# Kernel optimization log

Hardware: AMD Instinct MI355X
Metric: run time of the kernel (lower is better)

The kernel has to match this reference:

```python
import jax, jax.numpy as jnp
import numpy as np

DIM = 768
HEADS = 12
HEAD_DIM = DIM // HEADS
HIDDEN = 4 * DIM
EPS = 1e-5


def _ln(x, w, b):
    mu = jnp.mean(x, axis=-1, keepdims=True)
    var = jnp.var(x, axis=-1, keepdims=True)
    return (x - mu) * jax.lax.rsqrt(var + EPS) * w + b


def setup_inputs() -> dict:
    key = jax.random.key(0)
    ks = jax.random.split(key, 8)
    B, N, C = 8, 1024, DIM
    s = 0.02
    return {
        "before": jax.random.normal(ks[0], (B, N, C), jnp.float32),
        "after": jax.random.normal(ks[1], (B, N, C), jnp.float32),
        "norm1_w": jnp.ones((C,), jnp.float32),
        "norm1_b": jnp.zeros((C,), jnp.float32),
        "qkv_w": jax.random.normal(ks[2], (3 * C, C), jnp.float32) * s,
        "hln_w": jnp.ones((HEAD_DIM,), jnp.float32),
        "hln_b": jnp.zeros((HEAD_DIM,), jnp.float32),
        "proj_w": jax.random.normal(ks[3], (C, C), jnp.float32) * s,
        "proj_b": jnp.zeros((C,), jnp.float32),
        "norm2_w": jnp.ones((C,), jnp.float32),
        "norm2_b": jnp.zeros((C,), jnp.float32),
        "fc1_w": jax.random.normal(ks[4], (HIDDEN, C), jnp.float32) * s,
        "fc1_b": jnp.zeros((HIDDEN,), jnp.float32),
        "fc2_w": jax.random.normal(ks[5], (C, HIDDEN), jnp.float32) * s,
        "fc2_b": jnp.zeros((C,), jnp.float32),
    }


def _qkv_normed(x, qkv_w, hln_w, hln_b):
    B, N, C = x.shape
    qkv = x @ qkv_w.T  # (B,N,3C)
    qkv = qkv.reshape(B, N, 3, HEADS, HEAD_DIM).transpose(2, 0, 3, 1, 4)  # (3,B,H,N,hd)
    qkv = _ln(qkv, hln_w, hln_b)  # per-head LayerNorm over head_dim
    return qkv[0], qkv[1], qkv[2]


def _cross_attn(q, k, v, proj_w, proj_b):
    B, H, N, D = q.shape
    scale = D ** (-0.5)
    attn = jax.nn.softmax(jnp.einsum("bhnd,bhmd->bhnm", q, k) * scale, axis=-1)
    ctx = jnp.einsum("bhnm,bhmd->bhnd", attn, v)
    ctx = ctx.transpose(0, 2, 1, 3).reshape(B, N, H * D)
    ctx = ctx @ proj_w.T + proj_b
    # NOTE: original adds q.reshape(B,N,C) WITHOUT transposing heads (faithful)
    return ctx + q.reshape(B, N, H * D)


def _mlp(x, fc1_w, fc1_b, fc2_w, fc2_b):
    h = jax.nn.gelu(x @ fc1_w.T + fc1_b, approximate=False)
    return h @ fc2_w.T + fc2_b


def reference(before, after, norm1_w, norm1_b, qkv_w, hln_w, hln_b, proj_w, proj_b,
              norm2_w, norm2_b, fc1_w, fc1_b, fc2_w, fc2_b):
    before_n = _ln(before, norm1_w, norm1_b)
    after_n = _ln(after, norm1_w, norm1_b)
    q_b, k_b, v_b = _qkv_normed(before_n, qkv_w, hln_w, hln_b)
    q_a, k_a, v_a = _qkv_normed(after_n, qkv_w, hln_w, hln_b)
    context_a = _cross_attn(q_b, k_a, v_a, proj_w, proj_b)  # before attends to after
    context_b = _cross_attn(q_a, k_b, v_b, proj_w, proj_b)  # after attends to before
    before_o = before_n + context_b
    after_o = after_n + context_a
    before_o = before_o + _mlp(_ln(before_o, norm2_w, norm2_b), fc1_w, fc1_b, fc2_w, fc2_b)
    after_o = after_o + _mlp(_ln(after_o, norm2_w, norm2_b), fc1_w, fc1_b, fc2_w, fc2_b)
    return (before_o, after_o)
```

## Files before the change

### kernel.cpp

```cpp
#include <hip/hip_runtime.h>
#include <hip/hip_bf16.h>

typedef unsigned short u16;
typedef __attribute__((ext_vector_type(8))) short bf16x8;
typedef __attribute__((ext_vector_type(4))) float f32x4;

#define DIRSTRIDE 6291456

__device__ __forceinline__ u16 f2bf(float x){
  __hip_bfloat16 h = __float2bfloat16(x);
  return *reinterpret_cast<u16*>(&h);
}
__device__ __forceinline__ float bf2f(u16 u){
  return __uint_as_float(((unsigned int)u) << 16);
}
__device__ __forceinline__ u16 f2bf_fast(float x){
  return (u16)((__float_as_uint(x) + 0x8000u) >> 16);
}

__device__ __forceinline__ void xcd_remap(int& bx, int& by){
  int gx = (int)gridDim.x;
  int lin = (int)blockIdx.x + gx*(int)blockIdx.y;
  int nwg8 = (gx*(int)gridDim.y) >> 3;
  int rl = (lin & 7)*nwg8 + (lin >> 3);
  bx = rl % gx; by = rl / gx;
}

__global__ __launch_bounds__(256) void zero_kernel(float* __restrict__ p, int n){
  int i = blockIdx.x*256 + threadIdx.x;
  if (i < n) p[i] = 0.f;
}

__global__ __launch_bounds__(256) void cvt_kernel(const float* __restrict__ s,
                                                  u16* __restrict__ d, int n){
  int i = blockIdx.x*256 + threadIdx.x;
  if (i < n) d[i] = f2bf(s[i]);
}

__global__ __launch_bounds__(256) void ln_kernel(const float* __restrict__ s0,
    const float* __restrict__ s1, const float* __restrict__ w,
    const float* __restrict__ b, u16* __restrict__ out,
    float* __restrict__ mu_out, float* __restrict__ rs_out){
  int r = blockIdx.x;
  const float* src = (r < 8192) ? (s0 + (size_t)r*768) : (s1 + (size_t)(r-8192)*768);
  int t = threadIdx.x;
  float v0 = src[t], v1 = src[t+256], v2 = src[t+512];
  __shared__ float red[4];
  float s = v0+v1+v2;
  #pragma unroll
  for (int o=32;o;o>>=1) s += __shfl_xor(s,o);
  if ((t&63)==0) red[t>>6] = s;
  __syncthreads();
  float mean = (red[0]+red[1]+red[2]+red[3]) * (1.0f/768.0f);
  float d0=v0-mean, d1=v1-mean, d2=v2-mean;
  float q = d0*d0+d1*d1+d2*d2;
  __syncthreads();
  #pragma unroll
  for (int o=32;o;o>>=1) q += __shfl_xor(q,o);
  if ((t&63)==0) red[t>>6] = q;
  __syncthreads();
  float var = (red[0]+red[1]+red[2]+red[3]) * (1.0f/768.0f);
  float rstd = rsqrtf(var + 1e-5f);
  if (mu_out && t == 0){ mu_out[r] = mean; rs_out[r] = rstd; }
  size_t base = (size_t)r*768;
  out[base+t]     = f2bf(d0*rstd*w[t]     + b[t]);
  out[base+t+256] = f2bf(d1*rstd*w[t+256] + b[t+256]);
  out[base+t+512] = f2bf(d2*rstd*w[t+512] + b[t+512]);
}

__device__ __forceinline__ void stage_tile64(const u16* g, size_t strideK, u16* lds,
                                             int w, int lane){
  #pragma unroll
  for (int i=0;i<4;i++){
    int row = w*32 + i*8 + (lane>>3);
    int cs  = (lane&7) ^ (row&7);
    const u16* gp = g + (size_t)row*strideK + cs*8;
    __builtin_amdgcn_global_load_lds(
        (const __attribute__((address_space(1))) unsigned int*)gp,
        (__attribute__((address_space(3))) unsigned int*)(lds + (w*4+i)*512),
        16, 0, 0);
  }
}

__device__ __forceinline__ void stage_tile64x64(const u16* g, size_t strideK,
                                                u16* lds, int w, int lane){
  #pragma unroll
  for (int i=0;i<2;i++){
    int row = w*16 + i*8 + (lane>>3);
    int cs  = (lane&7) ^ (row&7);
    const u16* gp = g + (size_t)row*strideK + cs*8;
    __builtin_amdgcn_global_load_lds(
        (const __attribute__((address_space(1))) unsigned int*)gp,
        (__attribute__((address_space(3))) unsigned int*)(lds + (w*2+i)*512),
        16, 0, 0);
  }
}

#define SWZ_FRAG(tile, r, c) (*(const bf16x8*)&(tile)[(r)*64 + (((c) ^ ((r)&7)))*8])

template<int EPI>
__global__ __launch_bounds__(256, 4) void gemm_kernel(
    const u16* __restrict__ A, const u16* __restrict__ W, void* Cout,
    const float* __restrict__ bias, const float* resF,
    int M, int N, int K)
{
  __shared__ __attribute__((aligned(16))) u16 sA[128*64];
  __shared__ __attribute__((aligned(16))) u16 sB[128*64];
  int t = threadIdx.x;
  int w = t>>6, lane = t&63, ln = lane&15, quad = lane>>4;
  int bx, by; xcd_remap(bx, by);
  int m0 = by*128, n0 = bx*128;
  int wr = (w>>1)*64, wc = (w&1)*64;
  f32x4 acc[4][4];
  #pragma unroll
  for (int mi=0;mi<4;mi++)
    #pragma unroll
    for (int ni=0;ni<4;ni++) acc[mi][ni] = (f32x4){0.f,0.f,0.f,0.f};
  int KB = K >> 6;
  for (int kb=0;kb<KB;kb++){
    __syncthreads();
    stage_tile64(A + (size_t)m0*K + kb*64, K, sA, w, lane);
    stage_tile64(W + (size_t)n0*K + kb*64, K, sB, w, lane);
    __syncthreads();
    #pragma unroll
    for (int ks=0;ks<2;ks++){
      bf16x8 aF[4], bF[4];
      #pragma unroll
      for (int mi=0;mi<4;mi++) aF[mi] = SWZ_FRAG(sA, wr+mi*16+ln, ks*4+quad);
      #pragma unroll
      for (int ni=0;ni<4;ni++) bF[ni] = SWZ_FRAG(sB, wc+ni*16+ln, ks*4+quad);
      #pragma unroll
      for (int mi=0;mi<4;mi++)
        #pragma unroll
        for (int ni=0;ni<4;ni++)
          acc[mi][ni] = __builtin_amdgcn_mfma_f32_16x16x32_bf16(aF[mi], bF[ni], acc[mi][ni], 0,0,0);
    }
  }
  #pragma unroll
  for (int mi=0;mi<4;mi++){
    #pragma unroll
    for (int ni=0;ni<4;ni++){
      #pragma unroll
      for (int r=0;r<4;r++){
        int row = m0 + wr + mi*16 + quad*4 + r;
        int col = n0 + wc + ni*16 + ln;
        size_t ridx = (size_t)row*N + col;
        float v = acc[mi][ni][r];
        if (EPI == 2){
          v += bias[col];
          v = 0.5f*v*(1.0f + erff(v*0.70710678118654752f));
          ((u16*)Cout)[ridx] = f2bf(v);
        } else {
          float rf = resF[ridx];
          ((float*)Cout)[ridx] = v + bias[col] + rf;
        }
      }
    }
  }
}

__global__ __launch_bounds__(256, 4) void gemm_fc2_kernel(
    const u16* __restrict__ A, const u16* __restrict__ W, float* __restrict__ Cout,
    const float* __restrict__ bias, const float* resF)
{
  const int N = 768, K = 3072, KB = 48;
  __shared__ __attribute__((aligned(16))) u16 sA[128*64];
  __shared__ __attribute__((aligned(16))) u16 sB[64*64];
  int t = threadIdx.x;
  int w = t>>6, lane = t&63, ln = lane&15, quad = lane>>4;
  int bx, by; xcd_remap(bx, by);
  int m0 = by*128, n0 = bx*64;
  int wr = w*32;
  f32x4 acc[2][4];
  #pragma unroll
  for (int mi=0;mi<2;mi++)
    #pragma unroll
    for (int ni=0;ni<4;ni++) acc[mi][ni] = (f32x4){0.f,0.f,0.f,0.f};
  for (int kb=0;kb<KB;kb++){
    __syncthreads();
    stage_tile64(A + (size_t)m0*K + kb*64, K, sA, w, lane);
    stage_tile64x64(W + (size_t)n0*K + kb*64, K, sB, w, lane);
    __syncthreads();
    #pragma unroll
    for (int ks=0;ks<2;ks++){
      bf16x8 aF[2], bF[4];
      #pragma unroll
      for (int mi=0;mi<2;mi++) aF[mi] = SWZ_FRAG(sA, wr+mi*16+ln, ks*4+quad);
      #pragma unroll
      for (int ni=0;ni<4;ni++) bF[ni] = SWZ_FRAG(sB, ni*16+ln, ks*4+quad);
      #pragma unroll
      for (int mi=0;mi<2;mi++)
        #pragma unroll
        for (int ni=0;ni<4;ni++)
          acc[mi][ni] = __builtin_amdgcn_mfma_f32_16x16x32_bf16(aF[mi], bF[ni], acc[mi][ni], 0,0,0);
    }
  }
  #pragma unroll
  for (int mi=0;mi<2;mi++){
    #pragma unroll
    for (int ni=0;ni<4;ni++){
      #pragma unroll
      for (int r=0;r<4;r++){
        int row = m0 + wr + mi*16 + quad*4 + r;
        int col = n0 + ni*16 + ln;
        size_t ridx = (size_t)row*N + col;
        float rf = resF[ridx];
        Cout[ridx] = acc[mi][ni][r] + bias[col] + rf;
      }
    }
  }
}

__global__ __launch_bounds__(256, 4) void gemm_proj_kernel(
    const u16* __restrict__ A, const u16* __restrict__ W, float* Cout,
    const float* __restrict__ bias, const u16* __restrict__ resQ,
    const float* __restrict__ before, const float* __restrict__ after,
    const float* __restrict__ n1w, const float* __restrict__ n1b,
    const float* __restrict__ mu, const float* __restrict__ rstd)
{
  const int K = 768, N = 768, KB = 12;
  __shared__ __attribute__((aligned(16))) u16 sA[128*64];
  __shared__ __attribute__((aligned(16))) u16 sB[128*64];
  int t = threadIdx.x;
  int w = t>>6, lane = t&63, ln = lane&15, quad = lane>>4;
  int bx, by; xcd_remap(bx, by);
  int m0 = by*128, n0 = bx*128;
  int wr = (w>>1)*64, wc = (w&1)*64;
  f32x4 acc[4][4];
  #pragma unroll
  for (int mi=0;mi<4;mi++)
    #pragma unroll
    for (int ni=0;ni<4;ni++) acc[mi][ni] = (f32x4){0.f,0.f,0.f,0.f};
  for (int kb=0;kb<KB;kb++){
    __syncthreads();
    stage_tile64(A + (size_t)m0*K + kb*64, K, sA, w, lane);
    stage_tile64(W + (size_t)n0*K + kb*64, K, sB, w, lane);
    __syncthreads();
    #pragma unroll
    for (int ks=0;ks<2;ks++){
      bf16x8 aF[4], bF[4];
      #pragma unroll
      for (int mi=0;mi<4;mi++) aF[mi] = SWZ_FRAG(sA, wr+mi*16+ln, ks*4+quad);
      #pragma unroll
      for (int ni=0;ni<4;ni++) bF[ni] = SWZ_FRAG(sB, wc+ni*16+ln, ks*4+quad);
      #pragma unroll
      for (int mi=0;mi<4;mi++)
        #pragma unroll
        for (int ni=0;ni<4;ni++)
          acc[mi][ni] = __builtin_amdgcn_mfma_f32_16x16x32_bf16(aF[mi], bF[ni], acc[mi][ni], 0,0,0);
    }
  }
  #pragma unroll
  for (int mi=0;mi<4;mi++){
    #pragma unroll
    for (int ni=0;ni<4;ni++){
      #pragma unroll
      for (int r=0;r<4;r++){
        int row = m0 + wr + mi*16 + quad*4 + r;
        int col = n0 + wc + ni*16 + ln;
        size_t ridx = (size_t)row*N + col;
        int dirout = row >> 13;
        int rem = row & 8191;
        size_t qidx = (size_t)(1-dirout)*DIRSTRIDE + (size_t)rem*768 + col;
        const float* src = dirout ? after : before;
        float xr = (src[(size_t)rem*768 + col] - mu[row]) * rstd[row] * n1w[col] + n1b[col];
        Cout[ridx] = acc[mi][ni][r] + bias[col] + bf2f(resQ[qidx]) + xr;
      }
    }
  }
}

__global__ __launch_bounds__(256, 4) void gemm_qkv_kernel(
    const u16* __restrict__ A, const u16* __restrict__ W,
    const float* __restrict__ hw, const float* __restrict__ hb,
    u16* __restrict__ q, u16* __restrict__ k, u16* __restrict__ vt)
{
  const int K = 768, KB = 12;
  __shared__ __attribute__((aligned(16))) u16 sA[128*64];
  __shared__ __attribute__((aligned(16))) u16 sB[128*64];
  int t = threadIdx.x;
  int w = t>>6, lane = t&63, ln = lane&15, quad = lane>>4;
  int bx, by; xcd_remap(bx, by);
  int m0 = by*128, n0 = bx*128;
  int wr = (w>>1)*64, wc = (w&1)*64;
  f32x4 acc[4][4];
  #pragma unroll
  for (int mi=0;mi<4;mi++)
    #pragma unroll
    for (int ni=0;ni<4;ni++) acc[mi][ni] = (f32x4){0.f,0.f,0.f,0.f};
  for (int kb=0;kb<KB;kb++){
    __syncthreads();
    stage_tile64(A + (size_t)m0*K + kb*64, K, sA, w, lane);
    stage_tile64(W + (size_t)n0*K + kb*64, K, sB, w, lane);
    __syncthreads();
    #pragma unroll
    for (int ks=0;ks<2;ks++){
      bf16x8 aF[4], bF[4];
      #pragma unroll
      for (int mi=0;mi<4;mi++) aF[mi] = SWZ_FRAG(sA, wr+mi*16+ln, ks*4+quad);
      #pragma unroll
      for (int ni=0;ni<4;ni++) bF[ni] = SWZ_FRAG(sB, wc+ni*16+ln, ks*4+quad);
      #pragma unroll
      for (int mi=0;mi<4;mi++)
        #pragma unroll
        for (int ni=0;ni<4;ni++)
          acc[mi][ni] = __builtin_amdgcn_mfma_f32_16x16x32_bf16(aF[mi], bF[ni], acc[mi][ni], 0,0,0);
    }
  }
  int sec = (n0 + wc) >> 6;
  int which = sec / 12, h = sec - which*12;
  float hwv[4], hbv[4];
  #pragma unroll
  for (int ni=0;ni<4;ni++){ hwv[ni] = hw[ni*16+ln]; hbv[ni] = hb[ni*16+ln]; }
  #pragma unroll
  for (int mi=0;mi<4;mi++){
    #pragma unroll
    for (int r=0;r<4;r++){
      float s = acc[mi][0][r]+acc[mi][1][r]+acc[mi][2][r]+acc[mi][3][r];
      #pragma unroll
      for (int ofs=1; ofs<16; ofs<<=1) s += __shfl_xor(s, ofs);
      float mu = s * (1.0f/64.0f);
      float vv = 0.f;
      #pragma unroll
      for (int ni=0;ni<4;ni++){ float d = acc[mi][ni][r]-mu; vv += d*d; }
      #pragma unroll
      for (int ofs=1; ofs<16; ofs<<=1) vv += __shfl_xor(vv, ofs);
      float rstd = rsqrtf(vv*(1.0f/64.0f) + 1e-5f);
      int token = m0 + wr + mi*16 + quad*4 + r;
      int dir = token >> 13, bb = (token>>10)&7, n = token & 1023;
      size_t base = (size_t)dir*DIRSTRIDE + (size_t)bb*786432 + (size_t)h*65536;
      #pragma unroll
      for (int ni=0;ni<4;ni++){
        u16 y = f2bf((acc[mi][ni][r]-mu)*rstd*hwv[ni] + hbv[ni]);
        int hd = ni*16 + ln;
        if (which == 0)      q[base + (size_t)n*64 + hd] = y;
        else if (which == 1) k[base + (size_t)n*64 + hd] = y;
        else                 vt[base + (size_t)hd*1024 + n] = y;
      }
    }
  }
}

__global__ __launch_bounds__(256) void flash_kernel(const u16* __restrict__ qg,
    const u16* __restrict__ kg, const u16* __restrict__ vtg, u16* __restrict__ ctx)
{
  __shared__ __attribute__((aligned(16))) u16 sK[2][64*64];
  __shared__ __attribute__((aligned(16))) u16 sV[2][64*64];
  __shared__ __attribute__((aligned(16))) u16 sP[4*32*72];
  int lin = (int)blockIdx.x + 8*((int)blockIdx.y + 96*(int)blockIdx.z);
  int x8 = lin & 7, jj = lin >> 3;
  int qt = jj & 7;
  int g  = x8 + 8*(jj >> 3);
  int dout = g & 1, bh = g >> 1;
  int b = bh/12, h = bh - b*12;
  size_t qbase = (size_t)(1-dout)*DIRSTRIDE + (size_t)b*786432 + (size_t)h*65536;
  size_t kbase = (size_t)dout*DIRSTRIDE + (size_t)b*786432 + (size_t)h*65536;
  int t = threadIdx.x;
  int w = t>>6, lane = t&63, ln = lane&15, quad = lane>>4;
  const u16* qp = qg + qbase + (size_t)(qt*128 + w*32 + ln)*64 + quad*8;
  bf16x8 aQ[2][2];
  aQ[0][0] = *(const bf16x8*)qp;
  aQ[0][1] = *(const bf16x8*)(qp + 32);
  aQ[1][0] = *(const bf16x8*)(qp + 16*64);
  aQ[1][1] = *(const bf16x8*)(qp + 16*64 + 32);
  bf16x8 vOne;
  #pragma unroll
  for (int j=0;j<8;j++) vOne[j] = (short)0x3F80;
  f32x4 o[2][4], oL[2];
  #pragma unroll
  for (int mi=0;mi<2;mi++){
    #pragma unroll
    for (int ni=0;ni<4;ni++) o[mi][ni] = (f32x4){0.f,0.f,0.f,0.f};
    oL[mi] = (f32x4){0.f,0.f,0.f,0.f};
  }
  u16* pw = &sP[w*32*72];
  const float cs = 0.18033688011112042f;
  stage_tile64x64(kg  + kbase, 64, sK[0], w, lane);
  stage_tile64x64(vtg + kbase, 1024, sV[0], w, lane);
  __syncthreads();
  int cur = 0;
  for (int kt=0;kt<16;kt++){
    if (kt < 15){
      stage_tile64x64(kg  + kbase + (size_t)(kt+1)*4096, 64, sK[cur^1], w, lane);
      stage_tile64x64(vtg + kbase + (size_t)(kt+1)*64, 1024, sV[cur^1], w, lane);
    }
    const u16* sKc = sK[cur];
    const u16* sVc = sV[cur];
    bf16x8 bK[4][2];
    #pragma unroll
    for (int ni=0;ni<4;ni++){
      int rr = ni*16 + ln;
      bK[ni][0] = SWZ_FRAG(sKc, rr, quad);
      bK[ni][1] = SWZ_FRAG(sKc, rr, 4+quad);
    }
    f32x4 s[2][4];
    __builtin_amdgcn_s_setprio(1);
    #pragma unroll
    for (int mi=0;mi<2;mi++){
      #pragma unroll
      for (int ni=0;ni<4;ni++){
        s[mi][ni] = (f32x4){0.f,0.f,0.f,0.f};
        s[mi][ni] = __builtin_amdgcn_mfma_f32_16x16x32_bf16(aQ[mi][0], bK[ni][0], s[mi][ni], 0,0,0);
        s[mi][ni] = __builtin_amdgcn_mfma_f32_16x16x32_bf16(aQ[mi][1], bK[ni][1], s[mi][ni], 0,0,0);
      }
    }
    __builtin_amdgcn_s_setprio(0);
    bf16x8 bV[4][2];
    #pragma unroll
    for (int ni=0;ni<4;ni++){
      int rr = ni*16 + ln;
      bV[ni][0] = SWZ_FRAG(sVc, rr, quad);
      bV[ni][1] = SWZ_FRAG(sVc, rr, 4+quad);
    }
    #pragma unroll
    for (int mi=0;mi<2;mi++)
      #pragma unroll
      for (int ni=0;ni<4;ni++)
        #pragma unroll
        for (int r=0;r<4;r++){
          float p = exp2f(s[mi][ni][r]*cs);
          pw[(mi*16 + quad*4 + r)*72 + ni*16 + ln] = f2bf_fast(p);
        }
    bf16x8 aP[2][2];
    #pragma unroll
    for (int mi=0;mi<2;mi++){
      aP[mi][0] = *(const bf16x8*)&pw[(mi*16+ln)*72 + quad*8];
      aP[mi][1] = *(const bf16x8*)&pw[(mi*16+ln)*72 + 32 + quad*8];
    }
    __builtin_amdgcn_s_setprio(1);
    #pragma unroll
    for (int mi=0;mi<2;mi++){
      #pragma unroll
      for (int ni=0;ni<4;ni++){
        o[mi][ni] = __builtin_amdgcn_mfma_f32_16x16x32_bf16(aP[mi][0], bV[ni][0], o[mi][ni], 0,0,0);
        o[mi][ni] = __builtin_amdgcn_mfma_f32_16x16x32_bf16(aP[mi][1], bV[ni][1], o[mi][ni], 0,0,0);
      }
      oL[mi] = __builtin_amdgcn_mfma_f32_16x16x32_bf16(aP[mi][0], vOne, oL[mi], 0,0,0);
      oL[mi] = __builtin_amdgcn_mfma_f32_16x16x32_bf16(aP[mi][1], vOne, oL[mi], 0,0,0);
    }
    __builtin_amdgcn_s_setprio(0);
    __syncthreads();
    cur ^= 1;
  }
  #pragma unroll
  for (int mi=0;mi<2;mi++){
    #pragma unroll
    for (int r=0;r<4;r++){
      float inv = 1.0f / oL[mi][r];
      int row = qt*128 + w*32 + mi*16 + quad*4 + r;
      size_t obase = ((size_t)dout*8192 + (size_t)b*1024 + row)*768 + h*64;
      #pragma unroll
      for (int ni=0;ni<4;ni++)
        ctx[obase + ni*16 + ln] = f2bf(o[mi][ni][r] * inv);
    }
  }
}

extern "C" void kernel_launch(void* const* d_in, const int* in_sizes, int n_in,
                              void* d_out, int out_size, void* d_ws, size_t ws_size,
                              hipStream_t stream)
{
  const float* before = (const float*)d_in[0];
  const float* after  = (const float*)d_in[1];
  const float* n1w  = (const float*)d_in[2];
  const float* n1b  = (const float*)d_in[3];
  const float* qkvw = (const float*)d_in[4];
  const float* hlnw = (const float*)d_in[5];
  const float* hlnb = (const float*)d_in[6];
  const float* projw= (const float*)d_in[7];
  const float* projb= (const float*)d_in[8];
  const float* n2w  = (const float*)d_in[9];
  const float* n2b  = (const float*)d_in[10];
  const float* fc1w = (const float*)d_in[11];
  const float* fc1b = (const float*)d_in[12];
  const float* fc2w = (const float*)d_in[13];
  const float* fc2b = (const float*)d_in[14];

  const size_t REQUIRED = 114950144;
  if (ws_size < REQUIRED){
    zero_kernel<<<(out_size + 255)/256, 256, 0, stream>>>((float*)d_out, out_size);
    return;
  }

  char* ws = (char*)d_ws;
  u16* xn    = (u16*)(ws + 0);
  u16* ctxb  = (u16*)(ws + 0);
  u16* gbuf  = (u16*)(ws + 0);
  u16* qb    = (u16*)(ws + 25165824);
  u16* kb    = (u16*)(ws + 50331648);
  u16* h1n   = (u16*)(ws + 50331648);
  u16* vtb   = (u16*)(ws + 75497472);
  u16* wqkv  = (u16*)(ws + 100663296);
  u16* wproj = (u16*)(ws + 104202240);
  u16* wfc1  = (u16*)(ws + 105381888);
  u16* wfc2  = (u16*)(ws + 110100480);
  float* mu1  = (float*)(ws + 114819072);
  float* rs1  = (float*)(ws + 114884608);
  float* h1   = (float*)d_out;
  float* outp = (float*)d_out;

  cvt_kernel<<<6912, 256, 0, stream>>>(qkvw, wqkv, 1769472);
  cvt_kernel<<<2304, 256, 0, stream>>>(projw, wproj, 589824);
  cvt_kernel<<<9216, 256, 0, stream>>>(fc1w, wfc1, 2359296);
  cvt_kernel<<<9216, 256, 0, stream>>>(fc2w, wfc2, 2359296);

  ln_kernel<<<16384, 256, 0, stream>>>(before, after, n1w, n1b, xn, mu1, rs1);
  gemm_qkv_kernel<<<dim3(18,128), 256, 0, stream>>>(xn, wqkv, hlnw, hlnb, qb, kb, vtb);
  flash_kernel<<<dim3(8,96,2), 256, 0, stream>>>(qb, kb, vtb, ctxb);
  gemm_proj_kernel<<<dim3(6,128), 256, 0, stream>>>(ctxb, wproj, h1,
      projb, qb, before, after, n1w, n1b, mu1, rs1);
  ln_kernel<<<16384, 256, 0, stream>>>(h1, h1 + (size_t)8192*768, n2w, n2b, h1n,
      nullptr, nullptr);
  for (int c = 0; c < 2; c++){
    size_t off = (size_t)c * 8192 * 768;
    gemm_kernel<2><<<dim3(24,64), 256, 0, stream>>>(h1n + off, wfc1, gbuf,
        fc1b, nullptr, 8192, 3072, 768);
    gemm_fc2_kernel<<<dim3(12,64), 256, 0, stream>>>(gbuf, wfc2, outp + off,
        fc2b, h1 + off);
  }
}
```

Measured before the change: 617.3 us.

## Add double-buffered fc1 GEMM kernel and use raw exp in flash attention

Replaces the generic fc1 GEMM with a dedicated kernel that double-buffers 128x32 K-slices in LDS, so global-to-LDS loads of the next slice overlap the MFMAs on the current one. LDS use stays the same while load latency is hidden. Separately, flash attention swaps exp2f for a raw v_exp_f32 instruction and uses truncating-style fast bf16 conversion for the output, trimming ALU work. The raw exp skips denormal and range handling, which could slightly change precision.

```diff
diff --git a/kernel.cpp b/kernel.cpp
--- a/kernel.cpp
+++ b/kernel.cpp
@@ -16,6 +16,11 @@
 }
 __device__ __forceinline__ u16 f2bf_fast(float x){
   return (u16)((__float_as_uint(x) + 0x8000u) >> 16);
+}
+__device__ __forceinline__ float exp2_raw(float x){
+  float r;
+  asm("v_exp_f32 %0, %1" : "=v"(r) : "v"(x));
+  return r;
 }
 
 __device__ __forceinline__ void xcd_remap(int& bx, int& by){
@@ -96,7 +101,22 @@
   }
 }
 
+__device__ __forceinline__ void stage_tile32(const u16* g, size_t strideK,
+                                             u16* lds, int w, int lane){
+  #pragma unroll
+  for (int i=0;i<2;i++){
+    int row = w*32 + i*16 + (lane>>2);
+    int cs  = (lane&3) ^ ((lane>>3)&3);
+    const u16* gp = g + (size_t)row*strideK + cs*8;
+    __builtin_amdgcn_global_load_lds(
+        (const __attribute__((address_space(1))) unsigned int*)gp,
+        (__attribute__((address_space(3))) unsigned int*)(lds + (w*2+i)*512),
+        16, 0, 0);
+  }
+}
+
 #define SWZ_FRAG(tile, r, c) (*(const bf16x8*)&(tile)[(r)*64 + (((c) ^ ((r)&7)))*8])
+#define SWZ32(tile, r, c) (*(const bf16x8*)&(tile)[(r)*32 + (((c) ^ (((r)>>1)&3)))*8])
 
 template<int EPI>
 __global__ __launch_bounds__(256, 4) void gemm_kernel(
@@ -154,6 +174,69 @@
           float rf = resF[ridx];
           ((float*)Cout)[ridx] = v + bias[col] + rf;
         }
+      }
+    }
+  }
+}
+
+__global__ __launch_bounds__(256, 4) void gemm_fc1_kernel(
+    const u16* __restrict__ A, const u16* __restrict__ W, u16* __restrict__ Cout,
+    const float* __restrict__ bias)
+{
+  const int N = 3072, K = 768, KB = 24;
+  __shared__ __attribute__((aligned(16))) u16 sA[2][128*32];
+  __shared__ __attribute__((aligned(16))) u16 sB[2][128*32];
+  int t = threadIdx.x;
+  int w = t>>6, lane = t&63, ln = lane&15, quad = lane>>4;
+  int bx, by; xcd_remap(bx, by);
+  int m0 = by*128, n0 = bx*128;
+  int wr = (w>>1)*64, wc = (w&1)*64;
+  f32x4 acc[4][4];
+  #pragma unroll
+  for (int mi=0;mi<4;mi++)
+    #pragma unroll
+    for (int ni=0;ni<4;ni++) acc[mi][ni] = (f32x4){0.f,0.f,0.f,0.f};
+  stage_tile32(A + (size_t)m0*K, K, sA[0], w, lane);
+  stage_tile32(W + (size_t)n0*K, K, sB[0], w, lane);
+  int cur = 0;
+  for (int kb=0;kb<KB;kb++){
+    if (kb+1 < KB){
+      stage_tile32(A + (size_t)m0*K + (kb+1)*32, K, sA[cur^1], w, lane);
+      stage_tile32(W + (size_t)n0*K + (kb+1)*32, K, sB[cur^1], w, lane);
+      asm volatile("s_waitcnt vmcnt(4)" ::: "memory");
+    } else {
+      asm volatile("s_waitcnt vmcnt(0)" ::: "memory");
+    }
+    __builtin_amdgcn_s_barrier();
+    __builtin_amdgcn_sched_barrier(0);
+    const u16* pA = sA[cur];
+    const u16* pB = sB[cur];
+    bf16x8 aF[4], bF[4];
+    #pragma unroll
+    for (int mi=0;mi<4;mi++) aF[mi] = SWZ32(pA, wr+mi*16+ln, quad);
+    #pragma unroll
+    for (int ni=0;ni<4;ni++) bF[ni] = SWZ32(pB, wc+ni*16+ln, quad);
+    #pragma unroll
+    for (int mi=0;mi<4;mi++)
+      #pragma unroll
+      for (int ni=0;ni<4;ni++)
+        acc[mi][ni] = __builtin_amdgcn_mfma_f32_16x16x32_bf16(aF[mi], bF[ni], acc[mi][ni], 0,0,0);
+    __builtin_amdgcn_sched_barrier(0);
+    __builtin_amdgcn_s_barrier();
+    __builtin_amdgcn_sched_barrier(0);
+    cur ^= 1;
+  }
+  #pragma unroll
+  for (int mi=0;mi<4;mi++){
+    #pragma unroll
+    for (int ni=0;ni<4;ni++){
+      #pragma unroll
+      for (int r=0;r<4;r++){
+        int row = m0 + wr + mi*16 + quad*4 + r;
+        int col = n0 + wc + ni*16 + ln;
+        float v = acc[mi][ni][r] + bias[col];
+        v = 0.5f*v*(1.0f + erff(v*0.70710678118654752f));
+        Cout[(size_t)row*N + col] = f2bf(v);
       }
     }
   }
@@ -418,7 +501,7 @@
       for (int ni=0;ni<4;ni++)
         #pragma unroll
         for (int r=0;r<4;r++){
-          float p = exp2f(s[mi][ni][r]*cs);
+          float p = exp2_raw(s[mi][ni][r]*cs);
           pw[(mi*16 + quad*4 + r)*72 + ni*16 + ln] = f2bf_fast(p);
         }
     bf16x8 aP[2][2];
@@ -451,7 +534,7 @@
       size_t obase = ((size_t)dout*8192 + (size_t)b*1024 + row)*768 + h*64;
       #pragma unroll
       for (int ni=0;ni<4;ni++)
-        ctx[obase + ni*16 + ln] = f2bf(o[mi][ni][r] * inv);
+        ctx[obase + ni*16 + ln] = f2bf_fast(o[mi][ni][r] * inv);
     }
   }
 }
@@ -513,8 +596,7 @@
       nullptr, nullptr);
   for (int c = 0; c < 2; c++){
     size_t off = (size_t)c * 8192 * 768;
-    gemm_kernel<2><<<dim3(24,64), 256, 0, stream>>>(h1n + off, wfc1, gbuf,
-        fc1b, nullptr, 8192, 3072, 768);
+    gemm_fc1_kernel<<<dim3(24,64), 256, 0, stream>>>(h1n + off, wfc1, gbuf, fc1b);
     gemm_fc2_kernel<<<dim3(12,64), 256, 0, stream>>>(gbuf, wfc2, outp + off,
         fc2b, h1 + off);
   }
```

Measured after the change: 680.6 us. 10.3% more time.
